# Kernel tuning notes

Hardware: AMD Instinct MI355X
Metric: run time of the kernel (lower is better)

The kernel has to match this reference:

```python
import jax, jax.numpy as jnp
import numpy as np

HEADS = 8
HEAD_DIM = 64


def setup_inputs() -> dict:
    key = jax.random.key(0)
    ks = jax.random.split(key, 6)
    B, NQ, NC, D = 4, 1024, 8192, 512
    inner = HEADS * HEAD_DIM  # 512
    return {
        "x": jax.random.normal(ks[0], (B, NQ, D), dtype=jnp.float32),
        "context": jax.random.normal(ks[1], (B, NC, D), dtype=jnp.float32),
        "Wq": jax.random.normal(ks[2], (D, inner), dtype=jnp.float32) * (D ** -0.5),
        "Wkv": jax.random.normal(ks[3], (D, 2 * inner), dtype=jnp.float32) * (D ** -0.5),
        "Wout": jax.random.normal(ks[4], (inner, D), dtype=jnp.float32) * (inner ** -0.5),
        "bout": jax.random.normal(ks[5], (D,), dtype=jnp.float32) * 0.02,
    }


def reference(x, context, Wq, Wkv, Wout, bout):
    h, d = HEADS, HEAD_DIM
    scale = d ** -0.5
    b, nq, _ = x.shape
    nc = context.shape[1]
    q = x @ Wq                       # [b, nq, h*d]
    kv = context @ Wkv               # [b, nc, 2*h*d]
    k, v = jnp.split(kv, 2, axis=-1)
    # b n (h d) -> b h n d
    q = q.reshape(b, nq, h, d).transpose(0, 2, 1, 3)
    k = k.reshape(b, nc, h, d).transpose(0, 2, 1, 3)
    v = v.reshape(b, nc, h, d).transpose(0, 2, 1, 3)
    sim = jnp.einsum('bhid,bhjd->bhij', q, k) * scale  # [b, h, nq, nc]
    attn = jax.nn.softmax(sim, axis=-1)
    out = jnp.einsum('bhij,bhjd->bhid', attn, v)       # [b, h, nq, d]
    out = out.transpose(0, 2, 1, 3).reshape(b, nq, h * d)
    out = out @ Wout + bout          # [b, nq, queries_dim]
    return out.astype(x.dtype)
```

## Files before the change

### kernel.cpp

```cpp
#include <hip/hip_runtime.h>

#define B_   4
#define NQ_  1024
#define NC_  8192
#define D_   512
#define H_   8
#define HD_  64
#define NSPLIT 4
#define NCS  (NC_ / NSPLIT)

typedef __attribute__((ext_vector_type(4))) float f32x4;
typedef __attribute__((ext_vector_type(8))) short s16x8;
typedef __attribute__((ext_vector_type(4))) unsigned short u16x4;

__device__ inline unsigned short f2bf(float f) {
  unsigned int u = __float_as_uint(f);
  u += 0x7fffu + ((u >> 16) & 1u);
  return (unsigned short)(u >> 16);
}

#define GLL16(g, l)                                                            \
  __builtin_amdgcn_global_load_lds(                                            \
      (const __attribute__((address_space(1))) void*)(g),                      \
      (__attribute__((address_space(3))) void*)(l), 16, 0, 0)

__global__ void cvt_bf16(const float* __restrict__ in,
                         unsigned short* __restrict__ out, int n4) {
  int idx = blockIdx.x * blockDim.x + threadIdx.x;
  int stride = gridDim.x * blockDim.x;
  for (int i = idx; i < n4; i += stride) {
    float4 v = ((const float4*)in)[i];
    u16x4 o;
    o.x = f2bf(v.x); o.y = f2bf(v.y); o.z = f2bf(v.z); o.w = f2bf(v.w);
    *(u16x4*)&out[(long)i * 4] = o;
  }
}

__global__ void cvt_wT(const float* __restrict__ in,
                       unsigned short* __restrict__ out,
                       int K, int N, float scale) {
  int idx = blockIdx.x * 256 + threadIdx.x;
  if (idx < K * N) {
    int nn = idx / K, kk = idx - nn * K;
    out[idx] = f2bf(in[(long)kk * N + nn] * scale);
  }
}

template <int BM, int F32OUT>
__global__ __launch_bounds__(256, BM == 128 ? 2 : 4)
void gemm_bt(const unsigned short* __restrict__ A,
             const unsigned short* __restrict__ BT,
             void* __restrict__ C, const float* __restrict__ bias,
             int M, int N, int K) {
  constexpr int MR = BM / 32;
  __shared__ unsigned short As[BM * 32];
  __shared__ unsigned short Bs[BM * 32];
  const int tid = threadIdx.x;
  const int wid = tid >> 6;
  const int lane = tid & 63;
  const int l15 = lane & 15, l4 = lane >> 4;
  const int wr = wid >> 1, wc = wid & 1;
  const long brow = (long)blockIdx.y * BM;
  const long bcol = (long)blockIdx.x * BM;
  f32x4 acc[MR][MR] = {};

  for (int k0 = 0; k0 < K; k0 += 32) {
#pragma unroll
    for (int i = 0; i < BM / 64; ++i) {
      int c = i * 256 + tid;
      const unsigned short* ga = A  + (brow + (c >> 2)) * (long)K + k0 + (c & 3) * 8;
      const unsigned short* gb = BT + (bcol + (c >> 2)) * (long)K + k0 + (c & 3) * 8;
      GLL16(ga, (char*)As + i * 4096 + wid * 1024);
      GLL16(gb, (char*)Bs + i * 4096 + wid * 1024);
    }
    __syncthreads();
    s16x8 af[MR], bf[MR];
#pragma unroll
    for (int mi = 0; mi < MR; ++mi)
      af[mi] = *(const s16x8*)&As[(wr * (BM / 2) + mi * 16 + l15) * 32 + l4 * 8];
#pragma unroll
    for (int ni = 0; ni < MR; ++ni)
      bf[ni] = *(const s16x8*)&Bs[(wc * (BM / 2) + ni * 16 + l15) * 32 + l4 * 8];
#pragma unroll
    for (int mi = 0; mi < MR; ++mi)
#pragma unroll
      for (int ni = 0; ni < MR; ++ni)
        acc[mi][ni] = __builtin_amdgcn_mfma_f32_16x16x32_bf16(
            af[mi], bf[ni], acc[mi][ni], 0, 0, 0);
    __syncthreads();
  }

#pragma unroll
  for (int ni = 0; ni < MR; ++ni) {
    const long col = bcol + wc * (BM / 2) + ni * 16 + l15;
    float bv = 0.f;
    if (F32OUT) bv = bias[col];
#pragma unroll
    for (int mi = 0; mi < MR; ++mi) {
      const long row0 = brow + wr * (BM / 2) + mi * 16 + l4 * 4;
#pragma unroll
      for (int r = 0; r < 4; ++r) {
        float v = acc[mi][ni][r];
        if (F32OUT) ((float*)C)[(row0 + r) * N + col] = v + bv;
        else        ((unsigned short*)C)[(row0 + r) * N + col] = f2bf(v);
      }
    }
  }
}

__global__ __launch_bounds__(256, 2)
void vtrans(const unsigned short* __restrict__ kv,
            unsigned short* __restrict__ vt) {
  __shared__ unsigned short T[64 * 72];
  const int tid = threadIdx.x;
  const int bh = blockIdx.y, b = bh >> 3, h = bh & 7;
  const int nc0 = blockIdx.x * 64;
#pragma unroll
  for (int i = 0; i < 2; ++i) {
    int c = i * 256 + tid;
    int nc = c >> 3, dc = c & 7;
    s16x8 v = *(const s16x8*)&kv[((long)(b * NC_ + nc0 + nc)) * 1024 + 512 + h * 64 + dc * 8];
#pragma unroll
    for (int j = 0; j < 8; ++j)
      T[(dc * 8 + j) * 72 + nc] = (unsigned short)v[j];
  }
  __syncthreads();
#pragma unroll
  for (int i = 0; i < 2; ++i) {
    int c = i * 256 + tid;
    int d = c >> 3, ncc = c & 7;
    s16x8 t = *(const s16x8*)&T[d * 72 + ncc * 8];
    *(s16x8*)&vt[((long)(bh * 64 + d)) * NC_ + nc0 + ncc * 8] = t;
  }
}

__global__ __launch_bounds__(256, 6)
void attn_fwd(const unsigned short* __restrict__ q,
              const unsigned short* __restrict__ kv,
              const unsigned short* __restrict__ vt,
              float* __restrict__ Op, float* __restrict__ lp) {
  __shared__ unsigned short Ks[64 * 64];
  __shared__ unsigned short Vs[64 * 64];
  const int tid = threadIdx.x;
  const int wid = tid >> 6;
  const int lane = tid & 63;
  const int l15 = lane & 15, l4 = lane >> 4;
  const int bh = blockIdx.y, b = bh >> 3, h = bh & 7;
  const int q0 = blockIdx.x * 64;
  const int z = blockIdx.z;

  s16x8 qf[2];
  {
    const unsigned short* qrow =
        q + ((long)(b * NQ_ + q0 + wid * 16 + l15)) * 512 + h * 64;
#pragma unroll
    for (int ks = 0; ks < 2; ++ks)
      qf[ks] = *(const s16x8*)&qrow[ks * 32 + l4 * 8];
  }

  const int alo = (l15 + ((l4 & 1) << 5)) << 2;
  const int ahi = alo + 64;
  const int sel = l4 >> 1;

  float lrun = 0.f;
  f32x4 o[4] = {};

  for (int it = 0; it < NCS / 64; ++it) {
    const int nc0 = z * NCS + it * 64;
#pragma unroll
    for (int i = 0; i < 2; ++i) {
      int c = i * 256 + tid;
      int row = c >> 3;
      int colb = ((c & 7) * 16) ^ ((row & 7) << 4);
      const unsigned short* gk = kv + ((long)(b * NC_ + nc0 + row)) * 1024 + h * 64 + (colb >> 1);
      const unsigned short* gv = vt + ((long)(bh * 64 + row)) * NC_ + nc0 + (colb >> 1);
      GLL16(gk, (char*)Ks + i * 4096 + wid * 1024);
      GLL16(gv, (char*)Vs + i * 4096 + wid * 1024);
    }
    __syncthreads();

    f32x4 st[4] = {};
#pragma unroll
    for (int ks = 0; ks < 2; ++ks) {
#pragma unroll
      for (int ni = 0; ni < 4; ++ni) {
        int kvc = ni * 16 + l15;
        s16x8 kf = *(const s16x8*)((const char*)Ks + (kvc << 7) +
                                   (((ks * 64 + l4 * 16)) ^ ((kvc & 7) << 4)));
        st[ni] = __builtin_amdgcn_mfma_f32_16x16x32_bf16(kf, qf[ks], st[ni], 0, 0, 0);
      }
    }

    float p[4][4];
    float psum = 0.f;
#pragma unroll
    for (int ni = 0; ni < 4; ++ni)
#pragma unroll
      for (int r = 0; r < 4; ++r) {
        float v = __builtin_amdgcn_exp2f(st[ni][r]);
        p[ni][r] = v;
        psum += v;
      }
    lrun += psum;

    int pk[4][2];
#pragma unroll
    for (int ni = 0; ni < 4; ++ni)
#pragma unroll
      for (int u = 0; u < 2; ++u)
        asm("v_cvt_pk_bf16_f32 %0, %1, %2"
            : "=v"(pk[ni][u]) : "v"(p[ni][2 * u]), "v"(p[ni][2 * u + 1]));

#pragma unroll
    for (int ks = 0; ks < 2; ++ks) {
      int pw[4];
#pragma unroll
      for (int u = 0; u < 2; ++u) {
        int a0 = __builtin_amdgcn_ds_bpermute(alo, pk[2 * ks][u]);
        int b0 = __builtin_amdgcn_ds_bpermute(alo, pk[2 * ks + 1][u]);
        pw[u] = sel ? b0 : a0;
        int a1 = __builtin_amdgcn_ds_bpermute(ahi, pk[2 * ks][u]);
        int b1 = __builtin_amdgcn_ds_bpermute(ahi, pk[2 * ks + 1][u]);
        pw[2 + u] = sel ? b1 : a1;
      }
      s16x8 pa;
      __builtin_memcpy(&pa, pw, 16);
#pragma unroll
      for (int dn = 0; dn < 4; ++dn) {
        int d = dn * 16 + l15;
        s16x8 vf = *(const s16x8*)((const char*)Vs + (d << 7) +
                                   (((ks * 64 + l4 * 16)) ^ ((d & 7) << 4)));
        o[dn] = __builtin_amdgcn_mfma_f32_16x16x32_bf16(pa, vf, o[dn], 0, 0, 0);
      }
    }
    __syncthreads();
  }

  {
    float l0 = lrun;
    l0 += __shfl_xor(l0, 16, 64);
    l0 += __shfl_xor(l0, 32, 64);
    if (lane < 16)
      lp[((long)(z * 32 + bh)) * 1024 + q0 + wid * 16 + l15] = l0;
  }
#pragma unroll
  for (int dn = 0; dn < 4; ++dn)
#pragma unroll
    for (int r = 0; r < 4; ++r)
      Op[(((long)(z * 32 + bh)) * 1024 + q0 + wid * 16 + l4 * 4 + r) * 64 +
         dn * 16 + l15] = o[dn][r];
}

__global__ __launch_bounds__(256, 8)
void attn_combine(const float* __restrict__ Op, const float* __restrict__ lp,
                  unsigned short* __restrict__ att) {
  int idx = blockIdx.x * 256 + threadIdx.x;
  int col4 = idx & 127;
  int row = idx >> 7;
  int b = row >> 10, nq = row & 1023;
  int h = col4 >> 4, d4 = col4 & 15;
  float4 acc = {0.f, 0.f, 0.f, 0.f};
  float lsum = 0.f;
#pragma unroll
  for (int s = 0; s < NSPLIT; ++s) {
    const float4 v = *(const float4*)&Op[(((long)(s * 32 + b * 8 + h)) * 1024 + nq) * 64 + d4 * 4];
    acc.x += v.x; acc.y += v.y; acc.z += v.z; acc.w += v.w;
    lsum += lp[((long)(s * 32 + b * 8 + h)) * 1024 + nq];
  }
  float inv = 1.f / lsum;
  u16x4 o;
  o.x = f2bf(acc.x * inv); o.y = f2bf(acc.y * inv);
  o.z = f2bf(acc.z * inv); o.w = f2bf(acc.w * inv);
  *(u16x4*)&att[(long)row * 512 + col4 * 4] = o;
}

extern "C" void kernel_launch(void* const* d_in, const int* in_sizes, int n_in,
                              void* d_out, int out_size, void* d_ws, size_t ws_size,
                              hipStream_t stream) {
  (void)in_sizes; (void)n_in; (void)out_size; (void)ws_size;
  const float* x    = (const float*)d_in[0];
  const float* ctx  = (const float*)d_in[1];
  const float* Wq   = (const float*)d_in[2];
  const float* Wkv  = (const float*)d_in[3];
  const float* Wout = (const float*)d_in[4];
  const float* bout = (const float*)d_in[5];
  float* out = (float*)d_out;

  char* w = (char*)d_ws;
  unsigned short* x_bf   = (unsigned short*)w; w += (size_t)4096 * 512 * 2;
  unsigned short* ctx_bf = (unsigned short*)w; w += (size_t)32768 * 512 * 2;
  unsigned short* wqT    = (unsigned short*)w; w += (size_t)512 * 512 * 2;
  unsigned short* wkvT   = (unsigned short*)w; w += (size_t)1024 * 512 * 2;
  unsigned short* woutT  = (unsigned short*)w; w += (size_t)512 * 512 * 2;
  unsigned short* q_bf   = (unsigned short*)w; w += (size_t)4096 * 512 * 2;
  unsigned short* kv_bf  = (unsigned short*)w; w += (size_t)32768 * 1024 * 2;
  unsigned short* vt_bf  = (unsigned short*)w; w += (size_t)32 * 64 * NC_ * 2;
  unsigned short* att_bf = (unsigned short*)w; w += (size_t)4096 * 512 * 2;
  float* Opart = (float*)ctx_bf;
  float* lpart = (float*)x_bf;

  cvt_bf16<<<512,  256, 0, stream>>>(x,   x_bf,   4096 * 512 / 4);
  cvt_bf16<<<2048, 256, 0, stream>>>(ctx, ctx_bf, 32768 * 512 / 4);
  cvt_wT<<<1024, 256, 0, stream>>>(Wq,   wqT,   512, 512,  0.18033688f);
  cvt_wT<<<2048, 256, 0, stream>>>(Wkv,  wkvT,  512, 1024, 1.f);
  cvt_wT<<<1024, 256, 0, stream>>>(Wout, woutT, 512, 512,  1.f);

  gemm_bt<64, 0><<<dim3(8, 64),   256, 0, stream>>>(x_bf,   wqT,  q_bf,  nullptr, 4096,  512,  512);
  gemm_bt<128, 0><<<dim3(8, 256), 256, 0, stream>>>(ctx_bf, wkvT, kv_bf, nullptr, 32768, 1024, 512);
  vtrans<<<dim3(128, 32), 256, 0, stream>>>(kv_bf, vt_bf);
  attn_fwd<<<dim3(16, 32, NSPLIT), 256, 0, stream>>>(q_bf, kv_bf, vt_bf, Opart, lpart);
  attn_combine<<<2048, 256, 0, stream>>>(Opart, lpart, att_bf);
  gemm_bt<64, 1><<<dim3(8, 64), 256, 0, stream>>>(att_bf, woutT, out, bout, 4096, 512, 512);
}
```

Baseline: 349.0 us.

## Fuse V transpose into KV projection GEMM epilogue and drop vtrans kernel

The KV projection GEMM gains a mode that writes K rows into a compact 512-wide buffer and scatters V directly into the transposed per-head layout used by attention. This removes the separate vtrans kernel and the full write and read of V in the interleaved buffer. The direct transposed stores from the epilogue are narrow and strided, which may coalesce poorly. The attention kernel's launch bound occupancy hint is also raised.

```diff
diff --git a/kernel.cpp b/kernel.cpp
--- a/kernel.cpp
+++ b/kernel.cpp
@@ -46,11 +46,12 @@
   }
 }
 
-template <int BM, int F32OUT>
+template <int BM, int MODE>
 __global__ __launch_bounds__(256, BM == 128 ? 2 : 4)
 void gemm_bt(const unsigned short* __restrict__ A,
              const unsigned short* __restrict__ BT,
              void* __restrict__ C, const float* __restrict__ bias,
+             unsigned short* __restrict__ vt,
              int M, int N, int K) {
   constexpr int MR = BM / 32;
   __shared__ unsigned short As[BM * 32];
@@ -94,49 +95,33 @@
   for (int ni = 0; ni < MR; ++ni) {
     const long col = bcol + wc * (BM / 2) + ni * 16 + l15;
     float bv = 0.f;
-    if (F32OUT) bv = bias[col];
+    if (MODE == 1) bv = bias[col];
 #pragma unroll
     for (int mi = 0; mi < MR; ++mi) {
       const long row0 = brow + wr * (BM / 2) + mi * 16 + l4 * 4;
 #pragma unroll
       for (int r = 0; r < 4; ++r) {
+        const long row = row0 + r;
         float v = acc[mi][ni][r];
-        if (F32OUT) ((float*)C)[(row0 + r) * N + col] = v + bv;
-        else        ((unsigned short*)C)[(row0 + r) * N + col] = f2bf(v);
-      }
-    }
-  }
-}
-
-__global__ __launch_bounds__(256, 2)
-void vtrans(const unsigned short* __restrict__ kv,
-            unsigned short* __restrict__ vt) {
-  __shared__ unsigned short T[64 * 72];
-  const int tid = threadIdx.x;
-  const int bh = blockIdx.y, b = bh >> 3, h = bh & 7;
-  const int nc0 = blockIdx.x * 64;
-#pragma unroll
-  for (int i = 0; i < 2; ++i) {
-    int c = i * 256 + tid;
-    int nc = c >> 3, dc = c & 7;
-    s16x8 v = *(const s16x8*)&kv[((long)(b * NC_ + nc0 + nc)) * 1024 + 512 + h * 64 + dc * 8];
-#pragma unroll
-    for (int j = 0; j < 8; ++j)
-      T[(dc * 8 + j) * 72 + nc] = (unsigned short)v[j];
-  }
-  __syncthreads();
-#pragma unroll
-  for (int i = 0; i < 2; ++i) {
-    int c = i * 256 + tid;
-    int d = c >> 3, ncc = c & 7;
-    s16x8 t = *(const s16x8*)&T[d * 72 + ncc * 8];
-    *(s16x8*)&vt[((long)(bh * 64 + d)) * NC_ + nc0 + ncc * 8] = t;
-  }
-}
-
-__global__ __launch_bounds__(256, 6)
+        if (MODE == 1) ((float*)C)[row * N + col] = v + bv;
+        else if (MODE == 0) ((unsigned short*)C)[row * N + col] = f2bf(v);
+        else {
+          if (col < 512) {
+            ((unsigned short*)C)[row * 512 + col] = f2bf(v);
+          } else {
+            int b = (int)(row >> 13), nc = (int)(row & (NC_ - 1));
+            int hd = (int)col - 512;
+            vt[((long)(b * 8 + (hd >> 6)) * 64 + (hd & 63)) * NC_ + nc] = f2bf(v);
+          }
+        }
+      }
+    }
+  }
+}
+
+__global__ __launch_bounds__(256, 8)
 void attn_fwd(const unsigned short* __restrict__ q,
-              const unsigned short* __restrict__ kv,
+              const unsigned short* __restrict__ kq,
               const unsigned short* __restrict__ vt,
               float* __restrict__ Op, float* __restrict__ lp) {
   __shared__ unsigned short Ks[64 * 64];
@@ -172,8 +157,10 @@
       int c = i * 256 + tid;
       int row = c >> 3;
       int colb = ((c & 7) * 16) ^ ((row & 7) << 4);
-      const unsigned short* gk = kv + ((long)(b * NC_ + nc0 + row)) * 1024 + h * 64 + (colb >> 1);
-      const unsigned short* gv = vt + ((long)(bh * 64 + row)) * NC_ + nc0 + (colb >> 1);
+      const unsigned short* gk =
+          kq + ((long)(b * NC_ + nc0 + row)) * 512 + h * 64 + (colb >> 1);
+      const unsigned short* gv =
+          vt + ((long)(bh * 64 + row)) * NC_ + nc0 + (colb >> 1);
       GLL16(gk, (char*)Ks + i * 4096 + wid * 1024);
       GLL16(gv, (char*)Vs + i * 4096 + wid * 1024);
     }
@@ -293,7 +280,7 @@
   unsigned short* wkvT   = (unsigned short*)w; w += (size_t)1024 * 512 * 2;
   unsigned short* woutT  = (unsigned short*)w; w += (size_t)512 * 512 * 2;
   unsigned short* q_bf   = (unsigned short*)w; w += (size_t)4096 * 512 * 2;
-  unsigned short* kv_bf  = (unsigned short*)w; w += (size_t)32768 * 1024 * 2;
+  unsigned short* k_bf   = (unsigned short*)w; w += (size_t)32768 * 512 * 2;
   unsigned short* vt_bf  = (unsigned short*)w; w += (size_t)32 * 64 * NC_ * 2;
   unsigned short* att_bf = (unsigned short*)w; w += (size_t)4096 * 512 * 2;
   float* Opart = (float*)ctx_bf;
@@ -305,10 +292,12 @@
   cvt_wT<<<2048, 256, 0, stream>>>(Wkv,  wkvT,  512, 1024, 1.f);
   cvt_wT<<<1024, 256, 0, stream>>>(Wout, woutT, 512, 512,  1.f);
 
-  gemm_bt<64, 0><<<dim3(8, 64),   256, 0, stream>>>(x_bf,   wqT,  q_bf,  nullptr, 4096,  512,  512);
-  gemm_bt<128, 0><<<dim3(8, 256), 256, 0, stream>>>(ctx_bf, wkvT, kv_bf, nullptr, 32768, 1024, 512);
-  vtrans<<<dim3(128, 32), 256, 0, stream>>>(kv_bf, vt_bf);
-  attn_fwd<<<dim3(16, 32, NSPLIT), 256, 0, stream>>>(q_bf, kv_bf, vt_bf, Opart, lpart);
+  gemm_bt<64, 0><<<dim3(8, 64), 256, 0, stream>>>(
+      x_bf, wqT, q_bf, nullptr, nullptr, 4096, 512, 512);
+  gemm_bt<128, 2><<<dim3(8, 256), 256, 0, stream>>>(
+      ctx_bf, wkvT, k_bf, nullptr, vt_bf, 32768, 1024, 512);
+  attn_fwd<<<dim3(16, 32, NSPLIT), 256, 0, stream>>>(q_bf, k_bf, vt_bf, Opart, lpart);
   attn_combine<<<2048, 256, 0, stream>>>(Opart, lpart, att_bf);
-  gemm_bt<64, 1><<<dim3(8, 64), 256, 0, stream>>>(att_bf, woutT, out, bout, 4096, 512, 512);
-}
+  gemm_bt<64, 1><<<dim3(8, 64), 256, 0, stream>>>(
+      att_bf, woutT, out, bout, nullptr, 4096, 512, 512);
+}
```

Measured after the change: 384.3 us. 10.1% more time.
